# Optimization experiments

Hardware: AMD Instinct MI355X
Metric: run time of the kernel (lower is better)

The kernel has to match this reference:

```python
import jax, jax.numpy as jnp
import numpy as np

N_NODES = 50000
N_EDGES = 800000
IN_CH = 128
HID = 128


def _linear_params(key, fan_in, fan_out):
    kw, kb = jax.random.split(key)
    bound = 1.0 / np.sqrt(fan_in)
    W = jax.random.uniform(kw, (fan_in, fan_out), jnp.float32, -bound, bound)
    b = jax.random.uniform(kb, (fan_out,), jnp.float32, -bound, bound)
    return W, b


def setup_inputs() -> dict:
    key = jax.random.key(0)
    ks = jax.random.split(key, 11)
    x = jax.random.normal(ks[0], (N_NODES, IN_CH), jnp.float32)
    guidance_features = jax.random.normal(ks[1], (N_NODES, HID), jnp.float32)
    edge_index = jax.random.randint(ks[2], (2, N_EDGES), 0, N_NODES, jnp.int64)
    node_W, node_b = _linear_params(ks[3], IN_CH, HID)
    nbr_W, nbr_b = _linear_params(ks[4], IN_CH, HID)
    gud_W, gud_b = _linear_params(ks[5], HID, HID)
    enc_W, enc_b = _linear_params(ks[6], 3 * HID, HID)
    vp_W1, vp_b1 = _linear_params(ks[7], HID, HID // 2)
    vp_W2, vp_b2 = _linear_params(ks[8], HID // 2, 1)
    pol_W1, pol_b1 = _linear_params(ks[9], HID, HID)
    pol_W2, pol_b2 = _linear_params(ks[10], HID, 1)
    return dict(x=x, edge_index=edge_index, guidance_features=guidance_features,
                node_W=node_W, node_b=node_b, nbr_W=nbr_W, nbr_b=nbr_b,
                gud_W=gud_W, gud_b=gud_b, enc_W=enc_W, enc_b=enc_b,
                vp_W1=vp_W1, vp_b1=vp_b1, vp_W2=vp_W2, vp_b2=vp_b2,
                pol_W1=pol_W1, pol_b1=pol_b1, pol_W2=pol_W2, pol_b2=pol_b2)


def reference(x, edge_index, guidance_features,
              node_W, node_b, nbr_W, nbr_b, gud_W, gud_b,
              enc_W, enc_b, vp_W1, vp_b1, vp_W2, vp_b2,
              pol_W1, pol_b1, pol_W2, pol_b2):
    row, col = edge_index[0], edge_index[1]
    # Edge-wise gathers feeding three linear transforms -> [E, 3*HID] state
    node_feat = x[row] @ node_W + node_b            # [E, HID]
    nbr_feat = x[col] @ nbr_W + nbr_b               # [E, HID]
    gud_feat = guidance_features[col] @ gud_W + gud_b  # [E, HID]
    state = jnp.concatenate([node_feat, nbr_feat, gud_feat], axis=1)
    # state_encoder (eval mode: dropout = identity)
    enc = jax.nn.relu(state @ enc_W + enc_b)        # [E, HID]
    # value_predictor
    value_preds = jax.nn.relu(enc @ vp_W1 + vp_b1) @ vp_W2 + vp_b2  # [E, 1]
    # policy_net
    action_probs = jax.nn.sigmoid(
        jax.nn.relu(enc @ pol_W1 + pol_b1) @ pol_W2 + pol_b2)      # [E, 1]
    actions = (action_probs > 0.5).astype(x.dtype)  # eval-mode actions
    value_loss = jnp.zeros((), x.dtype)             # eval mode, labels=None
    return value_preds, action_probs, actions, value_loss
```

## Files before the change

kernel.cpp:

```cpp
#include <hip/hip_runtime.h>
#include <math.h>

#define N_NODES 50000
#define N_EDGES 800000

typedef __attribute__((ext_vector_type(8))) short short8_t;
typedef __attribute__((ext_vector_type(4))) float float4_t;

union U8 { short8_t v; unsigned short u[8]; };

__device__ __forceinline__ unsigned short bf16_rn(float f) {
    unsigned u = __float_as_uint(f);
    u += 0x7fffu + ((u >> 16) & 1u);
    return (unsigned short)(u >> 16);
}
__device__ __forceinline__ float bf2f(unsigned short h) {
    return __uint_as_float((unsigned)h << 16);
}
__device__ __forceinline__ void split3(float f, unsigned short& s0,
                                       unsigned short& s1, unsigned short& s2) {
    s0 = bf16_rn(f);  float r = f - bf2f(s0);
    s1 = bf16_rn(r);  r -= bf2f(s1);
    s2 = bf16_rn(r);
}
__device__ __forceinline__ void split3t(float f, unsigned short& s0,
                                        unsigned short& s1, unsigned short& s2) {
    unsigned u = __float_as_uint(f);
    s0 = (unsigned short)(u >> 16);
    float r = f - bf2f(s0);
    unsigned v = __float_as_uint(r);
    s1 = (unsigned short)(v >> 16);
    float r2 = r - bf2f(s1);
    s2 = bf16_rn(r2);
}


__global__ __launch_bounds__(256) void prep_kernel(
    const float* __restrict__ node_W, const float* __restrict__ node_b,
    const float* __restrict__ nbr_W,  const float* __restrict__ nbr_b,
    const float* __restrict__ gud_W,  const float* __restrict__ gud_b,
    const float* __restrict__ enc_W,  const float* __restrict__ enc_b,
    const float* __restrict__ vp_W1,  const float* __restrict__ vp_b1,
    const float* __restrict__ vp_W2,  const float* __restrict__ pol_W1,
    const float* __restrict__ pol_b1, const float* __restrict__ pol_W2,
    unsigned short* __restrict__ BTn0, unsigned short* __restrict__ BTn1,
    unsigned short* __restrict__ BTn2,
    unsigned short* __restrict__ BTg0, unsigned short* __restrict__ BTg1,
    unsigned short* __restrict__ BTg2,
    unsigned short* __restrict__ BTw0, unsigned short* __restrict__ BTw1,
    unsigned short* __restrict__ BTw2,
    float* __restrict__ cb, float* __restrict__ b1c, float* __restrict__ W2c,
    int* __restrict__ flags)
{
    const int k = blockIdx.x;
    const int j = threadIdx.x;
    if (j < 128) {
        float a = 0.f, b = 0.f;
        #pragma unroll 4
        for (int m = 0; m < 128; ++m) {
            a = fmaf(node_W[k * 128 + m], enc_W[m * 128 + j], a);
            b = fmaf(gud_W [k * 128 + m], enc_W[(256 + m) * 128 + j], b);
        }
        size_t i1 = (size_t)j * 128 + k;
        split3(a, BTn0[i1], BTn1[i1], BTn2[i1]);
        split3(b, BTg0[i1], BTg1[i1], BTg2[i1]);
    } else {
        const int n = j - 128;
        float a = 0.f;
        #pragma unroll 4
        for (int m = 0; m < 128; ++m)
            a = fmaf(nbr_W[k * 128 + m], enc_W[(128 + m) * 128 + n], a);
        size_t i2 = (size_t)(128 + n) * 128 + k;
        split3(a, BTn0[i2], BTn1[i2], BTn2[i2]);
    }
    if (j < 192) {
        float wv = (j < 64) ? vp_W1[k * 64 + j] : pol_W1[k * 128 + (j - 64)];
        size_t iw = (size_t)j * 128 + k;
        split3(wv, BTw0[iw], BTw1[iw], BTw2[iw]);
    }
    if (k == 0) {
        if (j < 128) {
            float cc = enc_b[j];
            for (int m = 0; m < 128; ++m) {
                cc = fmaf(node_b[m], enc_W[m * 128 + j], cc);
                cc = fmaf(nbr_b [m], enc_W[(128 + m) * 128 + j], cc);
                cc = fmaf(gud_b [m], enc_W[(256 + m) * 128 + j], cc);
            }
            cb[j] = cc;
        }
        if (j < 192) {
            b1c[j] = (j < 64) ? vp_b1[j] : pol_b1[j - 64];
            W2c[j] = (j < 64) ? vp_W2[j] : pol_W2[j - 64];
        }
        if (j < 64) {
            const int l = j, li = l & 15, lq = l >> 4;
            U8 A, B;
            #pragma unroll
            for (int u = 0; u < 8; ++u) { A.u[u] = 0; B.u[u] = 0; }
            if (lq == 0) {
                A.u[0] = bf16_rn((float)(li + 1));
                A.u[1] = bf16_rn(1.0f);
                B.u[0] = bf16_rn(1.0f);
                B.u[1] = bf16_rn((float)(100 * (li + 1)));
            }
            float4_t d = (float4_t){0.f, 0.f, 0.f, 0.f};
            d = __builtin_amdgcn_mfma_f32_16x16x32_bf16(A.v, B.v, d, 0, 0, 0);
            if (l == 17) {
                flags[0] = (fabsf(d[2] - 702.f) < 1.0f) ? 1 : 0;
            }
        }
    }
}

__global__ __launch_bounds__(256, 3) void node_kernel(
    const float* __restrict__ x, const float* __restrict__ g,
    const unsigned short* __restrict__ BTn0, const unsigned short* __restrict__ BTn1,
    const unsigned short* __restrict__ BTn2,
    const unsigned short* __restrict__ BTg0, const unsigned short* __restrict__ BTg1,
    const unsigned short* __restrict__ BTg2,
    const float* __restrict__ cb, const int* __restrict__ flags,
    float* __restrict__ P, float* __restrict__ Q)
{
    __shared__ unsigned short a0s[4 * 64 * 8];
    __shared__ unsigned short a1s[4 * 64 * 8];
    __shared__ unsigned short a2s[4 * 64 * 8];
    const int t = threadIdx.x;
    const int w = t >> 6, lane = t & 63;
    const int i16 = lane & 15, q = lane >> 4;
    const int base = blockIdx.x * 64;
    const int swap = flags[0];
    const int el = t >> 2, hh = t & 3;
    int nodeL = base + el; if (nodeL > N_NODES - 1) nodeL = N_NODES - 1;
    const float* xrow = x + (size_t)nodeL * 128 + hh * 8;
    const float* grow = g + (size_t)nodeL * 128 + hh * 8;

    float4_t acc[4][4];
    #pragma unroll
    for (int mt = 0; mt < 4; ++mt)
        #pragma unroll
        for (int nt = 0; nt < 4; ++nt) acc[mt][nt] = (float4_t){0.f, 0.f, 0.f, 0.f};

    float4 pv0 = *(const float4*)(xrow);
    float4 pv1 = *(const float4*)(xrow + 4);

    for (int kc = 0; kc < 8; ++kc) {
        U8 s0, s1, s2;
        {
            float e[8] = {pv0.x, pv0.y, pv0.z, pv0.w, pv1.x, pv1.y, pv1.z, pv1.w};
            #pragma unroll
            for (int u = 0; u < 8; ++u) split3t(e[u], s0.u[u], s1.u[u], s2.u[u]);
        }
        __syncthreads();
        {
            size_t off = ((size_t)hh * 64 + el) * 8;
            *(short8_t*)(a0s + off) = s0.v;
            *(short8_t*)(a1s + off) = s1.v;
            *(short8_t*)(a2s + off) = s2.v;
        }
        __syncthreads();
        if (kc < 7) {
            const float* nsrc = (kc + 1 < 4) ? (xrow + (kc + 1) * 32)
                                             : (grow + (kc + 1 - 4) * 32);
            pv0 = *(const float4*)(nsrc);
            pv1 = *(const float4*)(nsrc + 4);
        }
        if (kc < 4) {
            short8_t b0[4], b1v[4], b2v[4];
            #pragma unroll
            for (int ntl = 0; ntl < 4; ++ntl) {
                int ntg = w + ntl * 4;
                size_t roff = ((size_t)(ntg * 16 + i16)) * 128 + kc * 32 + q * 8;
                b0[ntl]  = *(const short8_t*)(BTn0 + roff);
                b1v[ntl] = *(const short8_t*)(BTn1 + roff);
                b2v[ntl] = *(const short8_t*)(BTn2 + roff);
            }
            #pragma unroll
            for (int mt = 0; mt < 4; ++mt) {
                size_t aoff = ((size_t)q * 64 + mt * 16 + i16) * 8;
                short8_t a0 = *(const short8_t*)(a0s + aoff);
                short8_t a1 = *(const short8_t*)(a1s + aoff);
                short8_t a2 = *(const short8_t*)(a2s + aoff);
                #pragma unroll
                for (int ntl = 0; ntl < 4; ++ntl) {
                    float4_t c = acc[mt][ntl];
                    c = __builtin_amdgcn_mfma_f32_16x16x32_bf16(a0, b0[ntl],  c, 0, 0, 0);
                    c = __builtin_amdgcn_mfma_f32_16x16x32_bf16(a0, b1v[ntl], c, 0, 0, 0);
                    c = __builtin_amdgcn_mfma_f32_16x16x32_bf16(a1, b0[ntl],  c, 0, 0, 0);
                    c = __builtin_amdgcn_mfma_f32_16x16x32_bf16(a0, b2v[ntl], c, 0, 0, 0);
                    c = __builtin_amdgcn_mfma_f32_16x16x32_bf16(a1, b1v[ntl], c, 0, 0, 0);
                    c = __builtin_amdgcn_mfma_f32_16x16x32_bf16(a2, b0[ntl],  c, 0, 0, 0);
                    acc[mt][ntl] = c;
                }
            }
        } else {
            short8_t b0[2], b1v[2], b2v[2];
            #pragma unroll
            for (int ntl = 0; ntl < 2; ++ntl) {
                int ntg = w + (ntl + 2) * 4;
                size_t roff = ((size_t)((ntg - 8) * 16 + i16)) * 128 + (kc - 4) * 32 + q * 8;
                b0[ntl]  = *(const short8_t*)(BTg0 + roff);
                b1v[ntl] = *(const short8_t*)(BTg1 + roff);
                b2v[ntl] = *(const short8_t*)(BTg2 + roff);
            }
            #pragma unroll
            for (int mt = 0; mt < 4; ++mt) {
                size_t aoff = ((size_t)q * 64 + mt * 16 + i16) * 8;
                short8_t a0 = *(const short8_t*)(a0s + aoff);
                short8_t a1 = *(const short8_t*)(a1s + aoff);
                short8_t a2 = *(const short8_t*)(a2s + aoff);
                #pragma unroll
                for (int ntl = 0; ntl < 2; ++ntl) {
                    float4_t c = acc[mt][ntl + 2];
                    c = __builtin_amdgcn_mfma_f32_16x16x32_bf16(a0, b0[ntl],  c, 0, 0, 0);
                    c = __builtin_amdgcn_mfma_f32_16x16x32_bf16(a0, b1v[ntl], c, 0, 0, 0);
                    c = __builtin_amdgcn_mfma_f32_16x16x32_bf16(a1, b0[ntl],  c, 0, 0, 0);
                    c = __builtin_amdgcn_mfma_f32_16x16x32_bf16(a0, b2v[ntl], c, 0, 0, 0);
                    c = __builtin_amdgcn_mfma_f32_16x16x32_bf16(a1, b1v[ntl], c, 0, 0, 0);
                    c = __builtin_amdgcn_mfma_f32_16x16x32_bf16(a2, b0[ntl],  c, 0, 0, 0);
                    acc[mt][ntl + 2] = c;
                }
            }
        }
    }

    if (!swap) {
        #pragma unroll
        for (int mt = 0; mt < 4; ++mt)
            #pragma unroll
            for (int ntl = 0; ntl < 4; ++ntl) {
                int ntg = w + ntl * 4;
                int chan = ntg * 16 + i16;
                bool isP = (ntg < 8);
                float bias = isP ? cb[chan] : 0.f;
                #pragma unroll
                for (int r = 0; r < 4; ++r) {
                    int node = base + mt * 16 + q * 4 + r;
                    if (node < N_NODES) {
                        if (isP) P[(size_t)node * 128 + chan] = acc[mt][ntl][r] + bias;
                        else     Q[(size_t)node * 128 + (chan - 128)] = acc[mt][ntl][r];
                    }
                }
            }
    } else {
        #pragma unroll
        for (int mt = 0; mt < 4; ++mt) {
            int node = base + mt * 16 + i16;
            if (node < N_NODES) {
                #pragma unroll
                for (int ntl = 0; ntl < 4; ++ntl) {
                    int ntg = w + ntl * 4;
                    int chanb = ntg * 16 + q * 4;
                    bool isP = (ntg < 8);
                    float4 vv;
                    vv.x = acc[mt][ntl][0] + (isP ? cb[chanb + 0] : 0.f);
                    vv.y = acc[mt][ntl][1] + (isP ? cb[chanb + 1] : 0.f);
                    vv.z = acc[mt][ntl][2] + (isP ? cb[chanb + 2] : 0.f);
                    vv.w = acc[mt][ntl][3] + (isP ? cb[chanb + 3] : 0.f);
                    if (isP) *(float4*)(P + (size_t)node * 128 + chanb) = vv;
                    else     *(float4*)(Q + (size_t)node * 128 + chanb - 128) = vv;
                }
            }
        }
    }
}

__global__ __launch_bounds__(256, 3) void edge_kernel(
    const int* __restrict__ ei,
    const float* __restrict__ P, const float* __restrict__ Q,
    const unsigned short* __restrict__ BTw0, const unsigned short* __restrict__ BTw1,
    const unsigned short* __restrict__ BTw2,
    const float* __restrict__ b1c, const float* __restrict__ W2c,
    const float* __restrict__ vp_b2, const float* __restrict__ pol_b2,
    const int* __restrict__ flags,
    float* __restrict__ out)
{
    __shared__ unsigned short enc0[4 * 64 * 8];
    __shared__ unsigned short enc1[4 * 64 * 8];
    __shared__ unsigned short enc2[4 * 64 * 8];
    __shared__ float vpart[256], ppart[256];

    const int t = threadIdx.x;
    const int w = t >> 6, lane = t & 63;
    const int i16 = lane & 15, q = lane >> 4;
    const int e0 = blockIdx.x * 64;
    const int ntg0 = w * 3;
    const int el = t >> 2, hh = t & 3;
    const int swap = flags[0];

    const int rowI = ei[e0 + el];
    const int colI = ei[N_EDGES + e0 + el];
    const float* Pp = P + (size_t)rowI * 128 + hh * 8;
    const float* Qp = Q + (size_t)colI * 128 + hh * 8;

    float4_t acc[4][3];
    #pragma unroll
    for (int mt = 0; mt < 4; ++mt)
        #pragma unroll
        for (int nt = 0; nt < 3; ++nt) acc[mt][nt] = (float4_t){0.f, 0.f, 0.f, 0.f};

    float4 pv0 = *(const float4*)(Pp);
    float4 pv1 = *(const float4*)(Pp + 4);
    float4 qv0 = *(const float4*)(Qp);
    float4 qv1 = *(const float4*)(Qp + 4);

    for (int kc = 0; kc < 4; ++kc) {
        U8 g0, g1, g2;
        {
            float ev[8] = {fmaxf(pv0.x + qv0.x, 0.f), fmaxf(pv0.y + qv0.y, 0.f),
                           fmaxf(pv0.z + qv0.z, 0.f), fmaxf(pv0.w + qv0.w, 0.f),
                           fmaxf(pv1.x + qv1.x, 0.f), fmaxf(pv1.y + qv1.y, 0.f),
                           fmaxf(pv1.z + qv1.z, 0.f), fmaxf(pv1.w + qv1.w, 0.f)};
            #pragma unroll
            for (int u = 0; u < 8; ++u) split3t(ev[u], g0.u[u], g1.u[u], g2.u[u]);
        }
        __syncthreads();
        {
            size_t off = ((size_t)hh * 64 + el) * 8;
            *(short8_t*)(enc0 + off) = g0.v;
            *(short8_t*)(enc1 + off) = g1.v;
            *(short8_t*)(enc2 + off) = g2.v;
        }
        __syncthreads();
        if (kc < 3) {
            pv0 = *(const float4*)(Pp + (kc + 1) * 32);
            pv1 = *(const float4*)(Pp + (kc + 1) * 32 + 4);
            qv0 = *(const float4*)(Qp + (kc + 1) * 32);
            qv1 = *(const float4*)(Qp + (kc + 1) * 32 + 4);
        }
        short8_t b0[3], b1f[3], b2f[3];
        #pragma unroll
        for (int ntl = 0; ntl < 3; ++ntl) {
            size_t roff = ((size_t)((ntg0 + ntl) * 16 + i16)) * 128 + kc * 32 + q * 8;
            b0[ntl]  = *(const short8_t*)(BTw0 + roff);
            b1f[ntl] = *(const short8_t*)(BTw1 + roff);
            b2f[ntl] = *(const short8_t*)(BTw2 + roff);
        }
        #pragma unroll
        for (int mt = 0; mt < 4; ++mt) {
            size_t aoff = ((size_t)q * 64 + mt * 16 + i16) * 8;
            short8_t a0 = *(const short8_t*)(enc0 + aoff);
            short8_t a1 = *(const short8_t*)(enc1 + aoff);
            short8_t a2 = *(const short8_t*)(enc2 + aoff);
            #pragma unroll
            for (int ntl = 0; ntl < 3; ++ntl) {
                float4_t c = acc[mt][ntl];
                c = __builtin_amdgcn_mfma_f32_16x16x32_bf16(a0, b0[ntl],  c, 0, 0, 0);
                c = __builtin_amdgcn_mfma_f32_16x16x32_bf16(a0, b1f[ntl], c, 0, 0, 0);
                c = __builtin_amdgcn_mfma_f32_16x16x32_bf16(a1, b0[ntl],  c, 0, 0, 0);
                c = __builtin_amdgcn_mfma_f32_16x16x32_bf16(a0, b2f[ntl], c, 0, 0, 0);
                c = __builtin_amdgcn_mfma_f32_16x16x32_bf16(a1, b1f[ntl], c, 0, 0, 0);
                c = __builtin_amdgcn_mfma_f32_16x16x32_bf16(a2, b0[ntl],  c, 0, 0, 0);
                acc[mt][ntl] = c;
            }
        }
    }

    if (!swap) {
        #pragma unroll
        for (int mt = 0; mt < 4; ++mt) {
            float vs[4] = {0.f, 0.f, 0.f, 0.f}, ps[4] = {0.f, 0.f, 0.f, 0.f};
            #pragma unroll
            for (int ntl = 0; ntl < 3; ++ntl) {
                int ntg = ntg0 + ntl;
                int n = ntg * 16 + i16;
                float b1s = b1c[n], w2s = W2c[n];
                bool isv = (ntg < 4);
                #pragma unroll
                for (int r = 0; r < 4; ++r) {
                    float hv = fmaxf(acc[mt][ntl][r] + b1s, 0.f) * w2s;
                    if (isv) vs[r] += hv; else ps[r] += hv;
                }
            }
            #pragma unroll
            for (int off = 1; off < 16; off <<= 1)
                #pragma unroll
                for (int r = 0; r < 4; ++r) {
                    vs[r] += __shfl_xor(vs[r], off, 64);
                    ps[r] += __shfl_xor(ps[r], off, 64);
                }
            if (i16 == 0)
                #pragma unroll
                for (int r = 0; r < 4; ++r) {
                    int eidx = mt * 16 + q * 4 + r;
                    vpart[w * 64 + eidx] = vs[r];
                    ppart[w * 64 + eidx] = ps[r];
                }
        }
    } else {
        #pragma unroll
        for (int mt = 0; mt < 4; ++mt) {
            float v = 0.f, p = 0.f;
            #pragma unroll
            for (int ntl = 0; ntl < 3; ++ntl) {
                int ntg = ntg0 + ntl;
                bool isv = (ntg < 4);
                #pragma unroll
                for (int r = 0; r < 4; ++r) {
                    int n = ntg * 16 + q * 4 + r;
                    float hv = fmaxf(acc[mt][ntl][r] + b1c[n], 0.f) * W2c[n];
                    if (isv) v += hv; else p += hv;
                }
            }
            v += __shfl_xor(v, 16, 64); v += __shfl_xor(v, 32, 64);
            p += __shfl_xor(p, 16, 64); p += __shfl_xor(p, 32, 64);
            if (q == 0) {
                int eidx = mt * 16 + i16;
                vpart[w * 64 + eidx] = v;
                ppart[w * 64 + eidx] = p;
            }
        }
    }
    __syncthreads();
    if (t < 64) {
        float v  = vpart[t] + vpart[64 + t] + vpart[128 + t] + vpart[192 + t] + vp_b2[0];
        float pl = ppart[t] + ppart[64 + t] + ppart[128 + t] + ppart[192 + t] + pol_b2[0];
        float prob = 1.0f / (1.0f + expf(-pl));
        int e = e0 + t;
        out[e] = v;
        out[N_EDGES + e] = prob;
        out[2 * N_EDGES + e] = (prob > 0.5f) ? 1.0f : 0.0f;
    }
    if (blockIdx.x == 0 && t == 0) out[3 * N_EDGES] = 0.0f;
}

extern "C" void kernel_launch(void* const* d_in, const int* in_sizes, int n_in,
                              void* d_out, int out_size, void* d_ws, size_t ws_size,
                              hipStream_t stream) {
    const float* x      = (const float*)d_in[0];
    const int*   ei     = (const int*)  d_in[1];
    const float* gf     = (const float*)d_in[2];
    const float* node_W = (const float*)d_in[3];
    const float* node_b = (const float*)d_in[4];
    const float* nbr_W  = (const float*)d_in[5];
    const float* nbr_b  = (const float*)d_in[6];
    const float* gud_W  = (const float*)d_in[7];
    const float* gud_b  = (const float*)d_in[8];
    const float* enc_W  = (const float*)d_in[9];
    const float* enc_b  = (const float*)d_in[10];
    const float* vp_W1  = (const float*)d_in[11];
    const float* vp_b1  = (const float*)d_in[12];
    const float* vp_W2  = (const float*)d_in[13];
    const float* vp_b2  = (const float*)d_in[14];
    const float* pol_W1 = (const float*)d_in[15];
    const float* pol_b1 = (const float*)d_in[16];
    const float* pol_W2 = (const float*)d_in[17];
    const float* pol_b2 = (const float*)d_in[18];
    float* out = (float*)d_out;

    unsigned char* wsb = (unsigned char*)d_ws;
    unsigned short* BTn0 = (unsigned short*)(wsb + 0);
    unsigned short* BTn1 = (unsigned short*)(wsb + 65536);
    unsigned short* BTn2 = (unsigned short*)(wsb + 131072);
    unsigned short* BTg0 = (unsigned short*)(wsb + 196608);
    unsigned short* BTg1 = (unsigned short*)(wsb + 229376);
    unsigned short* BTg2 = (unsigned short*)(wsb + 262144);
    unsigned short* BTw0 = (unsigned short*)(wsb + 294912);
    unsigned short* BTw1 = (unsigned short*)(wsb + 344064);
    unsigned short* BTw2 = (unsigned short*)(wsb + 393216);
    float* cb   = (float*)(wsb + 442368);
    float* b1c  = (float*)(wsb + 442880);
    float* W2c  = (float*)(wsb + 443648);
    int*   flags= (int*)  (wsb + 444416);
    float* Pd   = (float*)(wsb + 444480);
    float* Qd   = Pd + (size_t)N_NODES * 128;

    prep_kernel<<<dim3(128), dim3(256), 0, stream>>>(
        node_W, node_b, nbr_W, nbr_b, gud_W, gud_b, enc_W, enc_b,
        vp_W1, vp_b1, vp_W2, pol_W1, pol_b1, pol_W2,
        BTn0, BTn1, BTn2, BTg0, BTg1, BTg2, BTw0, BTw1, BTw2,
        cb, b1c, W2c, flags);

    node_kernel<<<dim3((N_NODES + 63) / 64), dim3(256), 0, stream>>>(
        x, gf, BTn0, BTn1, BTn2, BTg0, BTg1, BTg2, cb, flags, Pd, Qd);

    edge_kernel<<<dim3(N_EDGES / 64), dim3(256), 0, stream>>>(
        ei, Pd, Qd, BTw0, BTw1, BTw2, b1c, W2c, vp_b2, pol_b2, flags, out);
}
```

Baseline: 531.5 us.

## Make edge kernel persistent with LDS-resident weights and register-direct A fragments

The edge kernel becomes persistent: 256 blocks of 512 threads each load the full split-bf16 head weight matrix into 144KB of LDS once, pre-swizzled into MFMA fragment order by the prep kernel. Each wave now owns 16 edges and builds its A fragments straight from the gathered P/Q rows in registers, so the LDS staging and per-chunk __syncthreads are gone. Next-group gathers are software-prefetched across K-phases, and the epilogue writes outputs per wave instead of doing a cross-wave LDS reduction. The cost is one wave computing all 12 N-tiles, more registers per thread, and only 256 blocks, which may underfill the CUs and limit latency hiding.

```diff
diff --git a/kernel.cpp b/kernel.cpp
--- a/kernel.cpp
+++ b/kernel.cpp
@@ -3,6 +3,8 @@
 
 #define N_NODES 50000
 #define N_EDGES 800000
+#define EGRID 256
+#define EGROUPS 6250
 
 typedef __attribute__((ext_vector_type(8))) short short8_t;
 typedef __attribute__((ext_vector_type(4))) float float4_t;
@@ -47,8 +49,7 @@
     unsigned short* __restrict__ BTn2,
     unsigned short* __restrict__ BTg0, unsigned short* __restrict__ BTg1,
     unsigned short* __restrict__ BTg2,
-    unsigned short* __restrict__ BTw0, unsigned short* __restrict__ BTw1,
-    unsigned short* __restrict__ BTw2,
+    unsigned short* __restrict__ BTw_t,
     float* __restrict__ cb, float* __restrict__ b1c, float* __restrict__ W2c,
     int* __restrict__ flags)
 {
@@ -75,8 +76,11 @@
     }
     if (j < 192) {
         float wv = (j < 64) ? vp_W1[k * 64 + j] : pol_W1[k * 128 + (j - 64)];
-        size_t iw = (size_t)j * 128 + k;
-        split3(wv, BTw0[iw], BTw1[iw], BTw2[iw]);
+        const int kc = k >> 5, qq = (k >> 3) & 3, e = k & 7;
+        const int ntl = j >> 4, ii = j & 15;
+        size_t bidx = (size_t)((kc * 12 + ntl) * 3) * 512
+                    + (size_t)(qq * 16 + ii) * 8 + e;
+        split3(wv, BTw_t[bidx], BTw_t[bidx + 512], BTw_t[bidx + 1024]);
     }
     if (k == 0) {
         if (j < 128) {
@@ -264,163 +268,164 @@
     }
 }
 
-__global__ __launch_bounds__(256, 3) void edge_kernel(
+#define MFMA_PHASE(C)                                                           \
+    {                                                                           \
+        _Pragma("unroll")                                                       \
+        for (int n = 0; n < 12; ++n) {                                          \
+            const unsigned short* bp = Bl + ((C) * 12 + n) * 1536 + lane * 8;   \
+            short8_t b0  = *(const short8_t*)(bp);                              \
+            short8_t b1v = *(const short8_t*)(bp + 512);                        \
+            short8_t b2v = *(const short8_t*)(bp + 1024);                       \
+            float4_t cc = acc[n];                                               \
+            cc = __builtin_amdgcn_mfma_f32_16x16x32_bf16(a0.v, b0,  cc, 0, 0, 0); \
+            cc = __builtin_amdgcn_mfma_f32_16x16x32_bf16(a0.v, b1v, cc, 0, 0, 0); \
+            cc = __builtin_amdgcn_mfma_f32_16x16x32_bf16(a1.v, b0,  cc, 0, 0, 0); \
+            cc = __builtin_amdgcn_mfma_f32_16x16x32_bf16(a0.v, b2v, cc, 0, 0, 0); \
+            cc = __builtin_amdgcn_mfma_f32_16x16x32_bf16(a1.v, b1v, cc, 0, 0, 0); \
+            cc = __builtin_amdgcn_mfma_f32_16x16x32_bf16(a2.v, b0,  cc, 0, 0, 0); \
+            acc[n] = cc;                                                        \
+        }                                                                       \
+    }
+
+#define MAKE_FRAGS(P0, P1, Q0, Q1)                                              \
+    {                                                                           \
+        float ev[8] = {fmaxf((P0).x + (Q0).x, 0.f), fmaxf((P0).y + (Q0).y, 0.f),\
+                       fmaxf((P0).z + (Q0).z, 0.f), fmaxf((P0).w + (Q0).w, 0.f),\
+                       fmaxf((P1).x + (Q1).x, 0.f), fmaxf((P1).y + (Q1).y, 0.f),\
+                       fmaxf((P1).z + (Q1).z, 0.f), fmaxf((P1).w + (Q1).w, 0.f)};\
+        _Pragma("unroll")                                                       \
+        for (int u = 0; u < 8; ++u) split3t(ev[u], a0.u[u], a1.u[u], a2.u[u]);  \
+    }
+
+__global__ __launch_bounds__(512, 2) void edge_kernel(
     const int* __restrict__ ei,
     const float* __restrict__ P, const float* __restrict__ Q,
-    const unsigned short* __restrict__ BTw0, const unsigned short* __restrict__ BTw1,
-    const unsigned short* __restrict__ BTw2,
+    const unsigned short* __restrict__ BTw_t,
     const float* __restrict__ b1c, const float* __restrict__ W2c,
     const float* __restrict__ vp_b2, const float* __restrict__ pol_b2,
     const int* __restrict__ flags,
     float* __restrict__ out)
 {
-    __shared__ unsigned short enc0[4 * 64 * 8];
-    __shared__ unsigned short enc1[4 * 64 * 8];
-    __shared__ unsigned short enc2[4 * 64 * 8];
-    __shared__ float vpart[256], ppart[256];
+    extern __shared__ unsigned short Bl[];
 
     const int t = threadIdx.x;
     const int w = t >> 6, lane = t & 63;
     const int i16 = lane & 15, q = lane >> 4;
-    const int e0 = blockIdx.x * 64;
-    const int ntg0 = w * 3;
-    const int el = t >> 2, hh = t & 3;
     const int swap = flags[0];
 
-    const int rowI = ei[e0 + el];
-    const int colI = ei[N_EDGES + e0 + el];
-    const float* Pp = P + (size_t)rowI * 128 + hh * 8;
-    const float* Qp = Q + (size_t)colI * 128 + hh * 8;
-
-    float4_t acc[4][3];
     #pragma unroll
-    for (int mt = 0; mt < 4; ++mt)
-        #pragma unroll
-        for (int nt = 0; nt < 3; ++nt) acc[mt][nt] = (float4_t){0.f, 0.f, 0.f, 0.f};
-
-    float4 pv0 = *(const float4*)(Pp);
-    float4 pv1 = *(const float4*)(Pp + 4);
-    float4 qv0 = *(const float4*)(Qp);
-    float4 qv1 = *(const float4*)(Qp + 4);
-
-    for (int kc = 0; kc < 4; ++kc) {
-        U8 g0, g1, g2;
-        {
-            float ev[8] = {fmaxf(pv0.x + qv0.x, 0.f), fmaxf(pv0.y + qv0.y, 0.f),
-                           fmaxf(pv0.z + qv0.z, 0.f), fmaxf(pv0.w + qv0.w, 0.f),
-                           fmaxf(pv1.x + qv1.x, 0.f), fmaxf(pv1.y + qv1.y, 0.f),
-                           fmaxf(pv1.z + qv1.z, 0.f), fmaxf(pv1.w + qv1.w, 0.f)};
-            #pragma unroll
-            for (int u = 0; u < 8; ++u) split3t(ev[u], g0.u[u], g1.u[u], g2.u[u]);
-        }
-        __syncthreads();
-        {
-            size_t off = ((size_t)hh * 64 + el) * 8;
-            *(short8_t*)(enc0 + off) = g0.v;
-            *(short8_t*)(enc1 + off) = g1.v;
-            *(short8_t*)(enc2 + off) = g2.v;
-        }
-        __syncthreads();
-        if (kc < 3) {
-            pv0 = *(const float4*)(Pp + (kc + 1) * 32);
-            pv1 = *(const float4*)(Pp + (kc + 1) * 32 + 4);
-            qv0 = *(const float4*)(Qp + (kc + 1) * 32);
-            qv1 = *(const float4*)(Qp + (kc + 1) * 32 + 4);
-        }
-        short8_t b0[3], b1f[3], b2f[3];
-        #pragma unroll
-        for (int ntl = 0; ntl < 3; ++ntl) {
-            size_t roff = ((size_t)((ntg0 + ntl) * 16 + i16)) * 128 + kc * 32 + q * 8;
-            b0[ntl]  = *(const short8_t*)(BTw0 + roff);
-            b1f[ntl] = *(const short8_t*)(BTw1 + roff);
-            b2f[ntl] = *(const short8_t*)(BTw2 + roff);
-        }
-        #pragma unroll
-        for (int mt = 0; mt < 4; ++mt) {
-            size_t aoff = ((size_t)q * 64 + mt * 16 + i16) * 8;
-            short8_t a0 = *(const short8_t*)(enc0 + aoff);
-            short8_t a1 = *(const short8_t*)(enc1 + aoff);
-            short8_t a2 = *(const short8_t*)(enc2 + aoff);
-            #pragma unroll
-            for (int ntl = 0; ntl < 3; ++ntl) {
-                float4_t c = acc[mt][ntl];
-                c = __builtin_amdgcn_mfma_f32_16x16x32_bf16(a0, b0[ntl],  c, 0, 0, 0);
-                c = __builtin_amdgcn_mfma_f32_16x16x32_bf16(a0, b1f[ntl], c, 0, 0, 0);
-                c = __builtin_amdgcn_mfma_f32_16x16x32_bf16(a1, b0[ntl],  c, 0, 0, 0);
-                c = __builtin_amdgcn_mfma_f32_16x16x32_bf16(a0, b2f[ntl], c, 0, 0, 0);
-                c = __builtin_amdgcn_mfma_f32_16x16x32_bf16(a1, b1f[ntl], c, 0, 0, 0);
-                c = __builtin_amdgcn_mfma_f32_16x16x32_bf16(a2, b0[ntl],  c, 0, 0, 0);
-                acc[mt][ntl] = c;
-            }
-        }
-    }
-
-    if (!swap) {
-        #pragma unroll
-        for (int mt = 0; mt < 4; ++mt) {
-            float vs[4] = {0.f, 0.f, 0.f, 0.f}, ps[4] = {0.f, 0.f, 0.f, 0.f};
-            #pragma unroll
-            for (int ntl = 0; ntl < 3; ++ntl) {
-                int ntg = ntg0 + ntl;
-                int n = ntg * 16 + i16;
-                float b1s = b1c[n], w2s = W2c[n];
-                bool isv = (ntg < 4);
-                #pragma unroll
-                for (int r = 0; r < 4; ++r) {
-                    float hv = fmaxf(acc[mt][ntl][r] + b1s, 0.f) * w2s;
-                    if (isv) vs[r] += hv; else ps[r] += hv;
-                }
-            }
-            #pragma unroll
-            for (int off = 1; off < 16; off <<= 1)
-                #pragma unroll
-                for (int r = 0; r < 4; ++r) {
-                    vs[r] += __shfl_xor(vs[r], off, 64);
-                    ps[r] += __shfl_xor(ps[r], off, 64);
-                }
-            if (i16 == 0)
-                #pragma unroll
-                for (int r = 0; r < 4; ++r) {
-                    int eidx = mt * 16 + q * 4 + r;
-                    vpart[w * 64 + eidx] = vs[r];
-                    ppart[w * 64 + eidx] = ps[r];
-                }
-        }
-    } else {
-        #pragma unroll
-        for (int mt = 0; mt < 4; ++mt) {
-            float v = 0.f, p = 0.f;
-            #pragma unroll
-            for (int ntl = 0; ntl < 3; ++ntl) {
-                int ntg = ntg0 + ntl;
-                bool isv = (ntg < 4);
-                #pragma unroll
-                for (int r = 0; r < 4; ++r) {
-                    int n = ntg * 16 + q * 4 + r;
-                    float hv = fmaxf(acc[mt][ntl][r] + b1c[n], 0.f) * W2c[n];
-                    if (isv) v += hv; else p += hv;
-                }
-            }
-            v += __shfl_xor(v, 16, 64); v += __shfl_xor(v, 32, 64);
-            p += __shfl_xor(p, 16, 64); p += __shfl_xor(p, 32, 64);
-            if (q == 0) {
-                int eidx = mt * 16 + i16;
-                vpart[w * 64 + eidx] = v;
-                ppart[w * 64 + eidx] = p;
-            }
-        }
-    }
+    for (int i = 0; i < 18; ++i) {
+        int idx = (i * 512 + t) * 8;
+        *(short8_t*)(Bl + idx) = *(const short8_t*)(BTw_t + idx);
+    }
+    float b1r[12], w2r[12];
+    #pragma unroll
+    for (int n = 0; n < 12; ++n) {
+        b1r[n] = b1c[n * 16 + i16];
+        w2r[n] = W2c[n * 16 + i16];
+    }
+    const float vb2 = vp_b2[0], pb2 = pol_b2[0];
     __syncthreads();
-    if (t < 64) {
-        float v  = vpart[t] + vpart[64 + t] + vpart[128 + t] + vpart[192 + t] + vp_b2[0];
-        float pl = ppart[t] + ppart[64 + t] + ppart[128 + t] + ppart[192 + t] + pol_b2[0];
-        float prob = 1.0f / (1.0f + expf(-pl));
-        int e = e0 + t;
-        out[e] = v;
-        out[N_EDGES + e] = prob;
-        out[2 * N_EDGES + e] = (prob > 0.5f) ? 1.0f : 0.0f;
-    }
+
     if (blockIdx.x == 0 && t == 0) out[3 * N_EDGES] = 0.0f;
+
+    int grp = blockIdx.x;
+    {
+        int eg0 = grp * 128 + w * 16;
+        int rowI = ei[eg0 + i16];
+        int colI = ei[N_EDGES + eg0 + i16];
+        const float* Pp0 = P + (size_t)rowI * 128 + q * 8;
+        const float* Qp0 = Q + (size_t)colI * 128 + q * 8;
+        const float* Pp = Pp0;
+        const float* Qp = Qp0;
+        float4 pA0 = *(const float4*)(Pp);     float4 pA1 = *(const float4*)(Pp + 4);
+        float4 qA0 = *(const float4*)(Qp);     float4 qA1 = *(const float4*)(Qp + 4);
+        float4 pB0, pB1, qB0, qB1;
+
+        for (; grp < EGROUPS; grp += EGRID) {
+            const int eg = grp * 128 + w * 16;
+            float4_t acc[12];
+            #pragma unroll
+            for (int n = 0; n < 12; ++n) acc[n] = (float4_t){0.f, 0.f, 0.f, 0.f};
+
+            U8 a0, a1, a2;
+            const float *Ppn, *Qpn;
+
+            pB0 = *(const float4*)(Pp + 32);  pB1 = *(const float4*)(Pp + 36);
+            qB0 = *(const float4*)(Qp + 32);  qB1 = *(const float4*)(Qp + 36);
+            MAKE_FRAGS(pA0, pA1, qA0, qA1);
+            MFMA_PHASE(0);
+            pA0 = *(const float4*)(Pp + 64);  pA1 = *(const float4*)(Pp + 68);
+            qA0 = *(const float4*)(Qp + 64);  qA1 = *(const float4*)(Qp + 68);
+            MAKE_FRAGS(pB0, pB1, qB0, qB1);
+            MFMA_PHASE(1);
+            pB0 = *(const float4*)(Pp + 96);  pB1 = *(const float4*)(Pp + 100);
+            qB0 = *(const float4*)(Qp + 96);  qB1 = *(const float4*)(Qp + 100);
+            int gn = grp + EGRID; if (gn >= EGROUPS) gn = grp;
+            int egn = gn * 128 + w * 16;
+            int nrow = ei[egn + i16];
+            int ncol = ei[N_EDGES + egn + i16];
+            MAKE_FRAGS(pA0, pA1, qA0, qA1);
+            MFMA_PHASE(2);
+            Ppn = P + (size_t)nrow * 128 + q * 8;
+            Qpn = Q + (size_t)ncol * 128 + q * 8;
+            pA0 = *(const float4*)(Ppn);  pA1 = *(const float4*)(Ppn + 4);
+            qA0 = *(const float4*)(Qpn);  qA1 = *(const float4*)(Qpn + 4);
+            MAKE_FRAGS(pB0, pB1, qB0, qB1);
+            MFMA_PHASE(3);
+
+            if (!swap) {
+                float vs[4] = {0.f, 0.f, 0.f, 0.f}, ps[4] = {0.f, 0.f, 0.f, 0.f};
+                #pragma unroll
+                for (int n = 0; n < 12; ++n) {
+                    float b1s = b1r[n], w2s = w2r[n];
+                    #pragma unroll
+                    for (int r = 0; r < 4; ++r) {
+                        float hv = fmaxf(acc[n][r] + b1s, 0.f) * w2s;
+                        if (n < 4) vs[r] += hv; else ps[r] += hv;
+                    }
+                }
+                #pragma unroll
+                for (int off = 1; off < 16; off <<= 1)
+                    #pragma unroll
+                    for (int r = 0; r < 4; ++r) {
+                        vs[r] += __shfl_xor(vs[r], off, 64);
+                        ps[r] += __shfl_xor(ps[r], off, 64);
+                    }
+                if (i16 == 0) {
+                    #pragma unroll
+                    for (int r = 0; r < 4; ++r) {
+                        int e = eg + q * 4 + r;
+                        float prob = 1.0f / (1.0f + expf(-(ps[r] + pb2)));
+                        out[e] = vs[r] + vb2;
+                        out[N_EDGES + e] = prob;
+                        out[2 * N_EDGES + e] = (prob > 0.5f) ? 1.0f : 0.0f;
+                    }
+                }
+            } else {
+                float v = 0.f, p = 0.f;
+                #pragma unroll
+                for (int n = 0; n < 12; ++n)
+                    #pragma unroll
+                    for (int r = 0; r < 4; ++r) {
+                        int ch = n * 16 + q * 4 + r;
+                        float hv = fmaxf(acc[n][r] + b1c[ch], 0.f) * W2c[ch];
+                        if (n < 4) v += hv; else p += hv;
+                    }
+                v += __shfl_xor(v, 16, 64); v += __shfl_xor(v, 32, 64);
+                p += __shfl_xor(p, 16, 64); p += __shfl_xor(p, 32, 64);
+                if (q == 0) {
+                    int e = eg + i16;
+                    float prob = 1.0f / (1.0f + expf(-(p + pb2)));
+                    out[e] = v + vb2;
+                    out[N_EDGES + e] = prob;
+                    out[2 * N_EDGES + e] = (prob > 0.5f) ? 1.0f : 0.0f;
+                }
+            }
+
+            Pp = Ppn;  Qp = Qpn;
+        }
+    }
 }
 
 extern "C" void kernel_launch(void* const* d_in, const int* in_sizes, int n_in,
@@ -454,9 +459,7 @@
     unsigned short* BTg0 = (unsigned short*)(wsb + 196608);
     unsigned short* BTg1 = (unsigned short*)(wsb + 229376);
     unsigned short* BTg2 = (unsigned short*)(wsb + 262144);
-    unsigned short* BTw0 = (unsigned short*)(wsb + 294912);
-    unsigned short* BTw1 = (unsigned short*)(wsb + 344064);
-    unsigned short* BTw2 = (unsigned short*)(wsb + 393216);
+    unsigned short* BTw_t= (unsigned short*)(wsb + 294912);
     float* cb   = (float*)(wsb + 442368);
     float* b1c  = (float*)(wsb + 442880);
     float* W2c  = (float*)(wsb + 443648);
@@ -464,15 +467,23 @@
     float* Pd   = (float*)(wsb + 444480);
     float* Qd   = Pd + (size_t)N_NODES * 128;
 
+    static int attr_set = 0;
+    if (!attr_set) {
+        (void)hipFuncSetAttribute((const void*)edge_kernel,
+                                  hipFuncAttributeMaxDynamicSharedMemorySize,
+                                  147456);
+        attr_set = 1;
+    }
+
     prep_kernel<<<dim3(128), dim3(256), 0, stream>>>(
         node_W, node_b, nbr_W, nbr_b, gud_W, gud_b, enc_W, enc_b,
         vp_W1, vp_b1, vp_W2, pol_W1, pol_b1, pol_W2,
-        BTn0, BTn1, BTn2, BTg0, BTg1, BTg2, BTw0, BTw1, BTw2,
+        BTn0, BTn1, BTn2, BTg0, BTg1, BTg2, BTw_t,
         cb, b1c, W2c, flags);
 
     node_kernel<<<dim3((N_NODES + 63) / 64), dim3(256), 0, stream>>>(
         x, gf, BTn0, BTn1, BTn2, BTg0, BTg1, BTg2, cb, flags, Pd, Qd);
 
-    edge_kernel<<<dim3(N_EDGES / 64), dim3(256), 0, stream>>>(
-        ei, Pd, Qd, BTw0, BTw1, BTw2, b1c, W2c, vp_b2, pol_b2, flags, out);
-}
+    edge_kernel<<<dim3(EGRID), dim3(512), 147456, stream>>>(
+        ei, Pd, Qd, BTw_t, b1c, W2c, vp_b2, pol_b2, flags, out);
+}
```

Result: slower. 1.759 ms (+230.9%).
